# Performance work log

Measured on AMD Instinct MI355X. Metric: run time of the kernel, lower is better.

Reference implementation:

```python
import jax, jax.numpy as jnp
import numpy as np

EPS_IN = 1e-5  # torch InstanceNorm2d default eps


def _gather_nb(feat, idx):
    # feat: [B, C, N], idx: [B, M, K] -> [B, C, M, K]
    return jnp.take_along_axis(feat[:, :, :, None], idx[:, None, :, :], axis=2)


def _fc(x, w):
    # 1x1 conv2d: w [O, C], x [B, C, N, K] -> [B, O, N, K]
    return jnp.einsum('oc,bcnk->bonk', w, x)


def _inorm(x, w, b):
    # InstanceNorm2d(affine=True): per (batch, channel) stats over (N, K)
    mu = jnp.mean(x, axis=(2, 3), keepdims=True)
    var = jnp.var(x, axis=(2, 3), keepdims=True)
    xn = (x - mu) / jnp.sqrt(var + EPS_IN)
    return xn * w[None, :, None, None] + b[None, :, None, None]


def setup_inputs() -> dict:
    key = jax.random.key(0)
    ks = jax.random.split(key, 16)
    B, C_in, C_out, N, K = 8, 64, 64, 8192, 16
    x = jax.random.normal(ks[0], (B, C_in, N), dtype=jnp.float32)
    pos = jax.random.normal(ks[1], (B, 3, N), dtype=jnp.float32)
    support_points = jax.random.normal(ks[2], (B, 3, N), dtype=jnp.float32)
    neighbors_indices = jax.random.randint(ks[3], (B, N, K), 0, N)
    fc1_w = jax.random.normal(ks[4], (K, 3), dtype=jnp.float32) * 0.1
    fc2_w = jax.random.normal(ks[5], (K, 2 * K), dtype=jnp.float32) * 0.1
    fc3_w = jax.random.normal(ks[6], (K, 2 * K), dtype=jnp.float32) * 0.1
    bn1_w = jnp.ones((K,), jnp.float32)
    bn1_b = jnp.zeros((K,), jnp.float32)
    bn2_w = jnp.ones((K,), jnp.float32)
    bn2_b = jnp.zeros((K,), jnp.float32)
    cv_w = jax.random.normal(ks[7], (C_out, C_in, K), dtype=jnp.float32) * 0.05
    alpha = jnp.ones((1,), jnp.float32)
    beta = jnp.ones((1,), jnp.float32)
    return dict(x=x, pos=pos, support_points=support_points,
                neighbors_indices=neighbors_indices,
                fc1_w=fc1_w, fc2_w=fc2_w, fc3_w=fc3_w,
                bn1_w=bn1_w, bn1_b=bn1_b, bn2_w=bn2_w, bn2_b=bn2_b,
                cv_w=cv_w, alpha=alpha, beta=beta)


def reference(x, pos, support_points, neighbors_indices,
              fc1_w, fc2_w, fc3_w, bn1_w, bn1_b, bn2_w, bn2_b,
              cv_w, alpha, beta):
    K = neighbors_indices.shape[-1]
    pos_g = _gather_nb(pos, neighbors_indices)   # [B,3,N,K]
    x_g = _gather_nb(x, neighbors_indices)       # [B,C,N,K]
    pts = pos_g - support_points[:, :, :, None]  # [B,3,N,K]

    # adaptive normalization (eval mode; norm_radius == 1)
    d = jnp.sqrt(jnp.sum(jax.lax.stop_gradient(pts) ** 2, axis=1))  # [B,N,K]
    dw = jax.nn.sigmoid(-alpha[0] * d + beta[0])
    dws = jnp.sum(dw, axis=2, keepdims=True)
    dws = dws + (dws == 0).astype(dw.dtype) + 1e-6
    dw = (dw / dws * K)[:, None, :, :]           # [B,1,N,K]

    mat = jax.nn.relu(_inorm(_fc(pts, fc1_w), bn1_w, bn1_b))          # [B,K,N,K]
    mp1 = jnp.broadcast_to(jnp.max(mat * dw, axis=3, keepdims=True), mat.shape)
    mat = jnp.concatenate([mat, mp1], axis=1)
    mat = jax.nn.relu(_inorm(_fc(mat, fc2_w), bn2_w, bn2_b))
    mp2 = jnp.broadcast_to(jnp.max(mat * dw, axis=3, keepdims=True), mat.shape)
    mat = jnp.concatenate([mat, mp2], axis=1)
    mat = jax.nn.relu(_fc(mat, fc3_w)) * dw      # [B,Kk,N,K]

    # x.transpose(1,2) @ mat.permute(0,2,3,1): contract over neighbor axis k
    feats = jnp.einsum('bcnk,bjnk->bcnj', x_g, mat)  # [B,C,N,Kk]
    # Conv2d(in, out, (1, Kk)) then squeeze(3)
    out = jnp.einsum('ocj,bcnj->bon', cv_w, feats)   # [B,Cout,N]
    return out
```

## Files before the change

kernel.cpp:

```cpp
#include <hip/hip_runtime.h>
#include <cstdint>
#include <cstddef>

#define B_ 8
#define C_ 64
#define N_ 8192
#define K_ 16
#define CNT_ ((float)(N_ * K_))

typedef __attribute__((ext_vector_type(4))) float f32x4;
typedef __attribute__((ext_vector_type(8))) short short8;

union U8 { short8 v; unsigned u[4]; };

__device__ __forceinline__ unsigned pk2bf(float a, float b) {
    unsigned ua = __float_as_uint(a) + 0x8000u;
    unsigned ub = __float_as_uint(b) + 0x8000u;
    return __builtin_amdgcn_perm(ub, ua, 0x07060302u);
}
__device__ __forceinline__ unsigned short f2bf(float x) {
    return (unsigned short)((__float_as_uint(x) + 0x8000u) >> 16);
}
__device__ __forceinline__ float bflo(unsigned u) { return __uint_as_float(u << 16); }
__device__ __forceinline__ float bfhi(unsigned u) { return __uint_as_float(u & 0xffff0000u); }

template <int CTRL>
__device__ __forceinline__ float dppf(float v) {
    return __int_as_float(__builtin_amdgcn_update_dpp(0, __float_as_int(v), CTRL, 0xF, 0xF, true));
}
__device__ __forceinline__ float dpp_max16(float v) {
    v = fmaxf(v, dppf<0xB1>(v));
    v = fmaxf(v, dppf<0x4E>(v));
    v = fmaxf(v, dppf<0x141>(v));
    v = fmaxf(v, dppf<0x140>(v));
    return v;
}
__device__ __forceinline__ float dpp_add4(float v) {
    v += dppf<0xB1>(v);
    v += dppf<0x4E>(v);
    return v;
}
__device__ __forceinline__ float dpp_max4(float v) {
    v = fmaxf(v, dppf<0xB1>(v));
    v = fmaxf(v, dppf<0x4E>(v));
    return v;
}


__global__ __launch_bounds__(256) void k_pre(
    const float* __restrict__ cv, unsigned short* __restrict__ wf,
    const float* __restrict__ x, unsigned* __restrict__ xtb32, int use_xt,
    const float* __restrict__ pos, const float* __restrict__ sup,
    const int* __restrict__ nb, float* __restrict__ stats) {
    __shared__ float t[64][65];
    __shared__ float red[4][9];
    int tid = threadIdx.x;

    if (blockIdx.x < 256) {
        int g = blockIdx.x * 256 + tid;
        int e = g & 7, l = (g >> 3) & 63, w = (g >> 9) & 3, ks = g >> 11;
        int o = w * 16 + (l & 15);
        int i = ks * 32 + (l >> 4) * 8 + e;
        wf[g] = f2bf(cv[o * 1024 + i]);
        return;
    }
    int bid = blockIdx.x - 256;
    int b = bid >> 7, n0 = (bid & 127) << 6;

    if (use_xt) {
        int a = tid & 63, g = tid >> 6;
#pragma unroll
        for (int cc = 0; cc < 64; cc += 4)
            t[a][cc + g] = x[((size_t)b * 64 + cc + g) * N_ + n0 + a];
        __syncthreads();
        int cp = tid & 31, h = tid >> 5;
#pragma unroll
        for (int nn = 0; nn < 64; nn += 8) {
            int n = nn + h;
            xtb32[((size_t)b * N_ + n0 + n) * 32 + cp] = pk2bf(t[n][cp * 2], t[n][cp * 2 + 1]);
        }
    }

    {
        int n = n0 + (tid >> 2), q = tid & 3;
        size_t gn = (size_t)b * N_ + n;
        float sx = sup[(b * 3 + 0) * N_ + n];
        float sy = sup[(b * 3 + 1) * N_ + n];
        float sz = sup[(b * 3 + 2) * N_ + n];
        int4 ids = *(const int4*)&nb[gn * K_ + q * 4];
        const float* px_ = pos + (b * 3 + 0) * N_;
        const float* py_ = pos + (b * 3 + 1) * N_;
        const float* pz_ = pos + (b * 3 + 2) * N_;
        float Gx = 0.f, Gy = 0.f, Gz = 0.f;
        float Axx = 0.f, Ayy = 0.f, Azz = 0.f, Axy = 0.f, Axz = 0.f, Ayz = 0.f;
        int idk[4] = {ids.x, ids.y, ids.z, ids.w};
#pragma unroll
        for (int k = 0; k < 4; ++k) {
            int id = idk[k];
            float gx = px_[id], gy = py_[id], gz = pz_[id];
            Gx += gx; Gy += gy; Gz += gz;
            Axx = fmaf(gx, gx, Axx); Ayy = fmaf(gy, gy, Ayy); Azz = fmaf(gz, gz, Azz);
            Axy = fmaf(gx, gy, Axy); Axz = fmaf(gx, gz, Axz); Ayz = fmaf(gy, gz, Ayz);
        }
        float v[9];
        v[0] = Gx - 4.f * sx;
        v[1] = Gy - 4.f * sy;
        v[2] = Gz - 4.f * sz;
        v[3] = Axx - 2.f * sx * Gx + 4.f * sx * sx;
        v[4] = Ayy - 2.f * sy * Gy + 4.f * sy * sy;
        v[5] = Azz - 2.f * sz * Gz + 4.f * sz * sz;
        v[6] = Axy - sx * Gy - sy * Gx + 4.f * sx * sy;
        v[7] = Axz - sx * Gz - sz * Gx + 4.f * sx * sz;
        v[8] = Ayz - sy * Gz - sz * Gy + 4.f * sy * sz;
#pragma unroll
        for (int m = 1; m < 64; m <<= 1)
#pragma unroll
            for (int tt = 0; tt < 9; ++tt) v[tt] += __shfl_xor(v[tt], m);
        if ((tid & 63) == 0)
#pragma unroll
            for (int tt = 0; tt < 9; ++tt) red[tid >> 6][tt] = v[tt];
    }
    __syncthreads();
    if (tid < 9) {
        float s = red[0][tid] + red[1][tid] + red[2][tid] + red[3][tid];
        atomicAdd(&stats[b * 12 + tid], s);
    }
}

__global__ __launch_bounds__(256) void k_mid(
    const float* __restrict__ pos, const float* __restrict__ sup,
    const int* __restrict__ nb, const float* __restrict__ w1,
    const float* __restrict__ w2,
    const float* __restrict__ bn1w, const float* __restrict__ bn1b,
    const float* __restrict__ alpha, const float* __restrict__ beta,
    float* __restrict__ stats, unsigned* __restrict__ s2b,
    float* __restrict__ dwb, float* __restrict__ stats2, int store_s2) {
    __shared__ float sc1[16], sh1[16];
    __shared__ uint4 tile[4][64][4];
    __shared__ float redS[4][16], redQ[4][16];

    int tid = threadIdx.x;
    int wid = tid >> 6, l = tid & 63, hi = l >> 4, c15 = l & 15;
    int gn = blockIdx.x * 64 + (tid >> 2);
    int b = gn >> 13, n = gn & 8191, q = tid & 3;

    if (tid < 16) {
        int j = tid;
        const float* M = &stats[b * 12];
        float wx = w1[j * 3], wy = w1[j * 3 + 1], wz = w1[j * 3 + 2];
        float sum = wx * M[0] + wy * M[1] + wz * M[2];
        float sq = wx * wx * M[3] + wy * wy * M[4] + wz * wz * M[5]
                 + 2.f * (wx * wy * M[6] + wx * wz * M[7] + wy * wz * M[8]);
        float mu = sum / CNT_;
        float var = sq / CNT_ - mu * mu;
        float is = rsqrtf(var + 1e-5f);
        float sc = bn1w[j] * is;
        sc1[j] = sc;
        sh1[j] = bn1b[j] - mu * sc;
    }
    __syncthreads();

    union { short8 v; unsigned short u[8]; } af;
#pragma unroll
    for (int t = 0; t < 8; ++t) af.u[t] = f2bf(w2[c15 * 32 + hi * 8 + t]);

    float sx = sup[(b * 3 + 0) * N_ + n];
    float sy = sup[(b * 3 + 1) * N_ + n];
    float sz = sup[(b * 3 + 2) * N_ + n];
    int4 ids = *(const int4*)&nb[(size_t)gn * K_ + q * 4];
    int idk[4] = {ids.x, ids.y, ids.z, ids.w};

    float pxa[4], pya[4], pza[4], dwv[4];
    float dsum = 0.f;
    float al = alpha[0], be = beta[0];
#pragma unroll
    for (int k = 0; k < 4; ++k) {
        int id = idk[k];
        float px = pos[(b * 3 + 0) * N_ + id] - sx;
        float py = pos[(b * 3 + 1) * N_ + id] - sy;
        float pz = pos[(b * 3 + 2) * N_ + id] - sz;
        pxa[k] = px; pya[k] = py; pza[k] = pz;
        float d = sqrtf(px * px + py * py + pz * pz);
        float v = 1.f / (1.f + __expf(al * d - be));
        dwv[k] = v;
        dsum += v;
    }
    dsum = dpp_add4(dsum);
    float inv = 16.f / (dsum + (dsum == 0.f ? 1.f : 0.f) + 1e-6f);
#pragma unroll
    for (int k = 0; k < 4; ++k) dwv[k] *= inv;
    if (store_s2)
        *(float4*)&dwb[(size_t)gn * 16 + q * 4] = make_float4(dwv[0], dwv[1], dwv[2], dwv[3]);

    float mp1[16];
#pragma unroll
    for (int j = 0; j < 16; ++j) mp1[j] = 0.f;
    unsigned m1p[4][8];
#pragma unroll
    for (int t = 0; t < 4; ++t) {
        float px = pxa[t], py = pya[t], pz = pza[t], dw = dwv[t];
#pragma unroll
        for (int jp = 0; jp < 8; ++jp) {
            int j0 = 2 * jp, j1 = 2 * jp + 1;
            float v0 = fmaf(w1[j0 * 3 + 2], pz, fmaf(w1[j0 * 3 + 1], py, w1[j0 * 3] * px));
            float m0 = fmaxf(fmaf(v0, sc1[j0], sh1[j0]), 0.f);
            float v1 = fmaf(w1[j1 * 3 + 2], pz, fmaf(w1[j1 * 3 + 1], py, w1[j1 * 3] * px));
            float m1 = fmaxf(fmaf(v1, sc1[j1], sh1[j1]), 0.f);
            mp1[j0] = fmaxf(mp1[j0], m0 * dw);
            mp1[j1] = fmaxf(mp1[j1], m1 * dw);
            m1p[t][jp] = pk2bf(m0, m1);
        }
    }
#pragma unroll
    for (int j = 0; j < 16; ++j) mp1[j] = dpp_max4(mp1[j]);
    {
        unsigned mq[8];
#pragma unroll
        for (int t = 0; t < 8; ++t) mq[t] = pk2bf(mp1[2 * t], mp1[2 * t + 1]);
        tile[wid][l][2 ^ (l & 3)] = make_uint4(mq[0], mq[1], mq[2], mq[3]);
        tile[wid][l][3 ^ (l & 3)] = make_uint4(mq[4], mq[5], mq[6], mq[7]);
    }

    float ssum[4] = {0.f, 0.f, 0.f, 0.f}, ssq[4] = {0.f, 0.f, 0.f, 0.f};
    const f32x4 zero = {0.f, 0.f, 0.f, 0.f};

#pragma unroll
    for (int t = 0; t < 4; ++t) {
        tile[wid][l][0 ^ (l & 3)] = make_uint4(m1p[t][0], m1p[t][1], m1p[t][2], m1p[t][3]);
        tile[wid][l][1 ^ (l & 3)] = make_uint4(m1p[t][4], m1p[t][5], m1p[t][6], m1p[t][7]);
#pragma unroll
        for (int cg = 0; cg < 4; ++cg) {
            int e = cg * 16 + c15;
            union { uint4 u; short8 s; } bf;
            bf.u = tile[wid][e][hi ^ (e & 3)];
            f32x4 D = __builtin_amdgcn_mfma_f32_16x16x32_bf16(af.v, bf.s, zero, 0, 0, 0);
#pragma unroll
            for (int r = 0; r < 4; ++r) {
                ssum[r] += D[r];
                ssq[r] = fmaf(D[r], D[r], ssq[r]);
            }
            if (store_s2) {
                unsigned* tb = s2b + ((size_t)blockIdx.x * 64 + wid * 16 + cg * 4 + (c15 >> 2)) * 128;
                tb[t * 32 + (c15 & 3) * 8 + hi * 2 + 0] = pk2bf(D[0], D[1]);
                tb[t * 32 + (c15 & 3) * 8 + hi * 2 + 1] = pk2bf(D[2], D[3]);
            }
        }
    }
#pragma unroll
    for (int r = 0; r < 4; ++r) {
#pragma unroll
        for (int m = 1; m < 16; m <<= 1) {
            ssum[r] += __shfl_xor(ssum[r], m);
            ssq[r] += __shfl_xor(ssq[r], m);
        }
    }
    if (c15 == 0) {
#pragma unroll
        for (int r = 0; r < 4; ++r) { redS[wid][hi * 4 + r] = ssum[r]; redQ[wid][hi * 4 + r] = ssq[r]; }
    }
    __syncthreads();
    if (tid < 32) {
        int s = tid & 15;
        float v = (tid < 16) ? (redS[0][s] + redS[1][s] + redS[2][s] + redS[3][s])
                             : (redQ[0][s] + redQ[1][s] + redQ[2][s] + redQ[3][s]);
        if (store_s2) {
            atomicAdd(&stats2[(blockIdx.x & 7) * 256 + b * 32 + tid], v);
        } else {
            atomicAdd(&stats[(tid < 16 ? 256 : 384) + b * 16 + s], v);
        }
    }
}

template <int USE_XT, int USE_S2>
__global__ __launch_bounds__(256, 4) void k_main(
    const float* __restrict__ x, const unsigned short* __restrict__ xtb,
    const float* __restrict__ pos, const float* __restrict__ sup,
    const int* __restrict__ nb,
    const float* __restrict__ w1, const float* __restrict__ w2, const float* __restrict__ w3,
    const float* __restrict__ bn1w, const float* __restrict__ bn1b,
    const float* __restrict__ bn2w, const float* __restrict__ bn2b,
    const float* __restrict__ alpha, const float* __restrict__ beta,
    const unsigned short* __restrict__ wf,
    const float* __restrict__ stats,
    const unsigned* __restrict__ s2b, const float* __restrict__ dwb,
    const float* __restrict__ stats2,
    float* __restrict__ out) {
    __shared__ __align__(16) char lds_u[32768];
    int (*sidx)[4][16] = (int (*)[4][16])(lds_u + 16384);
    float* sc1 = (float*)(lds_u + 17408);
    float* sh1 = (float*)(lds_u + 17472);
    float* sc2 = (float*)(lds_u + 17536);
    float* sh2 = (float*)(lds_u + 17600);

    int tid = threadIdx.x;
    int b = blockIdx.x & 7;
    int n0 = (blockIdx.x >> 3) << 4;
    int wid = tid >> 6, l = tid & 63, hi = l >> 4, c15 = l & 15;
    int hi2 = hi >> 1;
    const f32x4 zero = {0.f, 0.f, 0.f, 0.f};

    {
        int n = n0 + wid * 4 + hi;
        sidx[wid][hi][c15] = nb[((size_t)b * N_ + n) * K_ + c15];
    }

    unsigned G0[4][4], G1[4][4];
    if constexpr (USE_XT) {
        const unsigned short* xb = xtb + (size_t)b * N_ * 64;
#pragma unroll
        for (int pi = 0; pi < 4; ++pi) {
            int4 ids = *(const int4*)&sidx[wid][pi][hi * 4];
            int idr[4] = {ids.x, ids.y, ids.z, ids.w};
#pragma unroll
            for (int r = 0; r < 4; ++r) {
                uint2 g = *(const uint2*)(xb + (size_t)idr[r] * 64 + c15 * 4);
                G0[pi][r] = g.x; G1[pi][r] = g.y;
            }
        }
    }

    uint2 sv[4];
    float dwc[4];
    if constexpr (USE_S2) {
#pragma unroll
        for (int eg = 0; eg < 4; ++eg) {
            size_t gn_e = (size_t)b * N_ + n0 + wid * 4 + eg;
            sv[eg] = *(const uint2*)&s2b[gn_e * 128 + (c15 & 3) * 32 + (c15 >> 2) * 8 + hi * 2];
            dwc[eg] = dwb[gn_e * 16 + c15];
        }
    }

    if constexpr (USE_S2) {
        if (tid < 32) {
            float acc = 0.f;
#pragma unroll
            for (int c = 0; c < 8; ++c) acc += stats2[c * 256 + b * 32 + tid];
            float sq = __shfl(acc, (tid & 15) + 16);
            if (tid < 16) {
                float mu = acc / CNT_;
                float var = sq / CNT_ - mu * mu;
                float is = rsqrtf(var + 1e-5f);
                float sc = bn2w[tid] * is;
                sc2[tid] = sc;
                sh2[tid] = bn2b[tid] - mu * sc;
            }
        }
    } else if (tid < 32) {
        int j = tid & 15, set = tid >> 4;
        float mu, var;
        if (set == 0) {
            const float* M = &stats[b * 12];
            float wx = w1[j * 3], wy = w1[j * 3 + 1], wz = w1[j * 3 + 2];
            float sum = wx * M[0] + wy * M[1] + wz * M[2];
            float sq = wx * wx * M[3] + wy * wy * M[4] + wz * wz * M[5]
                     + 2.f * (wx * wy * M[6] + wx * wz * M[7] + wy * wz * M[8]);
            mu = sum / CNT_;
            var = sq / CNT_ - mu * mu;
        } else {
            float su = stats[256 + b * 16 + j];
            float sq = stats[384 + b * 16 + j];
            mu = su / CNT_;
            var = sq / CNT_ - mu * mu;
        }
        float is = rsqrtf(var + 1e-5f);
        float wv = set ? bn2w[j] : bn1w[j];
        float bv = set ? bn2b[j] : bn1b[j];
        float scale = wv * is;
        if (set == 0) { sc1[j] = scale; sh1[j] = bv - mu * scale; }
        else          { sc2[j] = scale; sh2[j] = bv - mu * scale; }
    }
    __syncthreads();

    U8 w3f;
    {
        const float* wp = w3 + c15 * 32 + hi * 8;
        w3f.u[0] = pk2bf(wp[0], wp[1]); w3f.u[1] = pk2bf(wp[2], wp[3]);
        w3f.u[2] = pk2bf(wp[4], wp[5]); w3f.u[3] = pk2bf(wp[6], wp[7]);
    }
    float sc2r[4], sh2r[4];
#pragma unroll
    for (int r = 0; r < 4; ++r) { sc2r[r] = sc2[hi * 4 + r]; sh2r[r] = sh2[hi * 4 + r]; }

    char* tw = lds_u + (wid << 12);

    float m2v[4][4];
    if constexpr (USE_S2) {
#pragma unroll
        for (int eg = 0; eg < 4; ++eg) {
            m2v[eg][0] = fmaxf(fmaf(bflo(sv[eg].x), sc2r[0], sh2r[0]), 0.f);
            m2v[eg][1] = fmaxf(fmaf(bfhi(sv[eg].x), sc2r[1], sh2r[1]), 0.f);
            m2v[eg][2] = fmaxf(fmaf(bflo(sv[eg].y), sc2r[2], sh2r[2]), 0.f);
            m2v[eg][3] = fmaxf(fmaf(bfhi(sv[eg].y), sc2r[3], sh2r[3]), 0.f);
        }
    } else {
        U8 w2f;
        {
            const float* wp = w2 + c15 * 32 + hi * 8;
            w2f.u[0] = pk2bf(wp[0], wp[1]); w2f.u[1] = pk2bf(wp[2], wp[3]);
            w2f.u[2] = pk2bf(wp[4], wp[5]); w2f.u[3] = pk2bf(wp[6], wp[7]);
        }
        float dw;
        {
            int p_e = wid * 4 + hi;
            int n = n0 + p_e;
            int id = sidx[wid][hi][c15];
            float px = pos[(b * 3 + 0) * N_ + id] - sup[(b * 3 + 0) * N_ + n];
            float py = pos[(b * 3 + 1) * N_ + id] - sup[(b * 3 + 1) * N_ + n];
            float pz = pos[(b * 3 + 2) * N_ + id] - sup[(b * 3 + 2) * N_ + n];
            float d = sqrtf(px * px + py * py + pz * pz);
            float dwr = 1.f / (1.f + __expf(alpha[0] * d - beta[0]));
            float dws = dwr;
            dws += __shfl_xor(dws, 1); dws += __shfl_xor(dws, 2);
            dws += __shfl_xor(dws, 4); dws += __shfl_xor(dws, 8);
            dws += (dws == 0.f ? 1.f : 0.f) + 1e-6f;
            dw = dwr * 16.f / dws;

            float m1[16];
#pragma unroll
            for (int j = 0; j < 16; ++j) {
                float v = fmaf(w1[j * 3 + 2], pz, fmaf(w1[j * 3 + 1], py, w1[j * 3] * px));
                m1[j] = fmaxf(fmaf(v, sc1[j], sh1[j]), 0.f);
            }
            float mp1[16];
#pragma unroll
            for (int j = 0; j < 16; ++j) {
                float t = m1[j] * dw;
                t = fmaxf(t, __shfl_xor(t, 1)); t = fmaxf(t, __shfl_xor(t, 2));
                t = fmaxf(t, __shfl_xor(t, 4)); t = fmaxf(t, __shfl_xor(t, 8));
                mp1[j] = t;
            }
            int swz = (l >> 1) & 7;
            uint4 q0 = make_uint4(pk2bf(m1[0], m1[1]), pk2bf(m1[2], m1[3]), pk2bf(m1[4], m1[5]), pk2bf(m1[6], m1[7]));
            uint4 q1 = make_uint4(pk2bf(m1[8], m1[9]), pk2bf(m1[10], m1[11]), pk2bf(m1[12], m1[13]), pk2bf(m1[14], m1[15]));
            uint4 q2 = make_uint4(pk2bf(mp1[0], mp1[1]), pk2bf(mp1[2], mp1[3]), pk2bf(mp1[4], mp1[5]), pk2bf(mp1[6], mp1[7]));
            uint4 q3 = make_uint4(pk2bf(mp1[8], mp1[9]), pk2bf(mp1[10], mp1[11]), pk2bf(mp1[12], mp1[13]), pk2bf(mp1[14], mp1[15]));
            ((uint4*)tw)[(l * 4 + 0) ^ swz] = q0;
            ((uint4*)tw)[(l * 4 + 1) ^ swz] = q1;
            ((uint4*)tw)[(l * 4 + 2) ^ swz] = q2;
            ((uint4*)tw)[(l * 4 + 3) ^ swz] = q3;
        }
#pragma unroll
        for (int eg = 0; eg < 4; ++eg) {
            int e = eg * 16 + c15;
            uint4 t = ((const uint4*)tw)[(e * 4 + hi) ^ (c15 >> 1)];
            U8 bf; bf.u[0] = t.x; bf.u[1] = t.y; bf.u[2] = t.z; bf.u[3] = t.w;
            f32x4 D2 = __builtin_amdgcn_mfma_f32_16x16x32_bf16(w2f.v, bf.v, zero, 0, 0, 0);
            dwc[eg] = __shfl(dw, eg * 16 + c15);
#pragma unroll
            for (int r = 0; r < 4; ++r)
                m2v[eg][r] = fmaxf(fmaf(D2[r], sc2r[r], sh2r[r]), 0.f);
        }
    }

#pragma unroll
    for (int eg = 0; eg < 4; ++eg) {
        float mp2v[4];
#pragma unroll
        for (int r = 0; r < 4; ++r)
            mp2v[r] = dpp_max16(m2v[eg][r] * dwc[eg]);
        uint2 mq = make_uint2(pk2bf(m2v[eg][0], m2v[eg][1]), pk2bf(m2v[eg][2], m2v[eg][3]));
        uint2 pq = make_uint2(pk2bf(mp2v[0], mp2v[1]), pk2bf(mp2v[2], mp2v[3]));
        int e = eg * 16 + c15, sw = c15 >> 1;
        ((uint2*)tw)[(e * 8 + hi) ^ sw] = mq;
        ((uint2*)tw)[(e * 8 + 4 + hi) ^ sw] = pq;
    }

    f32x4 D3[4];
#pragma unroll
    for (int eg = 0; eg < 4; ++eg) {
        int e = eg * 16 + c15, sw = c15 >> 1;
        uint2 b0 = ((const uint2*)tw)[(e * 8 + hi * 2) ^ sw];
        uint2 b1 = ((const uint2*)tw)[(e * 8 + hi * 2 + 1) ^ sw];
        U8 bf; bf.u[0] = b0.x; bf.u[1] = b0.y; bf.u[2] = b1.x; bf.u[3] = b1.y;
        D3[eg] = __builtin_amdgcn_mfma_f32_16x16x32_bf16(w3f.v, bf.v, zero, 0, 0, 0);
    }

#pragma unroll
    for (int eg = 0; eg < 4; ++eg) {
#pragma unroll
        for (int r = 0; r < 4; ++r) {
            float v = fmaxf(D3[eg][r], 0.f) * dwc[eg];
            ((unsigned short*)(tw + eg * 640))[(hi * 4 + r) * 20 + c15] = f2bf(v);
        }
    }

    uint2 afr2[4];
#pragma unroll
    for (int pi = 0; pi < 4; ++pi)
        afr2[pi] = *(const uint2*)(tw + pi * 640 + c15 * 40 + hi * 8);

    uint2 dv[4][4];
    if constexpr (USE_XT) {
#pragma unroll
        for (int pi = 0; pi < 4; ++pi) {
            U8 av; av.u[0] = afr2[pi].x; av.u[1] = afr2[pi].y; av.u[2] = 0; av.u[3] = 0;
#pragma unroll
            for (int cg = 0; cg < 4; ++cg) {
                unsigned w0 = (cg < 2) ? G0[pi][0] : G1[pi][0];
                unsigned w1_ = (cg < 2) ? G0[pi][1] : G1[pi][1];
                unsigned w2_ = (cg < 2) ? G0[pi][2] : G1[pi][2];
                unsigned w3_ = (cg < 2) ? G0[pi][3] : G1[pi][3];
                unsigned sel = (cg & 1) ? 0x07060302u : 0x05040100u;
                U8 bf;
                bf.u[0] = __builtin_amdgcn_perm(w1_, w0, sel);
                bf.u[1] = __builtin_amdgcn_perm(w3_, w2_, sel);
                bf.u[2] = 0; bf.u[3] = 0;
                f32x4 D = __builtin_amdgcn_mfma_f32_16x16x32_bf16(av.v, bf.v, zero, 0, 0, 0);
                dv[pi][cg] = make_uint2(pk2bf(D[0], D[1]), pk2bf(D[2], D[3]));
            }
        }
    } else {
#pragma unroll
        for (int pi = 0; pi < 4; ++pi) {
            int4 ids = *(const int4*)&sidx[wid][pi][hi * 4];
            U8 av; av.u[0] = afr2[pi].x; av.u[1] = afr2[pi].y; av.u[2] = 0; av.u[3] = 0;
#pragma unroll
            for (int cg = 0; cg < 4; ++cg) {
                int c = cg * 16 + c15;
                const float* xc = x + ((size_t)b * 64 + c) * N_;
                U8 bf;
                bf.u[0] = pk2bf(xc[ids.x], xc[ids.y]);
                bf.u[1] = pk2bf(xc[ids.z], xc[ids.w]);
                bf.u[2] = 0; bf.u[3] = 0;
                f32x4 D = __builtin_amdgcn_mfma_f32_16x16x32_bf16(av.v, bf.v, zero, 0, 0, 0);
                dv[pi][cg] = make_uint2(pk2bf(D[0], D[1]), pk2bf(D[2], D[3]));
            }
        }
    }

    __syncthreads();

    const unsigned short* wbase = wf + (size_t)wid * 512 + (size_t)l * 8;
    U8 aW[4];
#pragma unroll
    for (int i = 0; i < 4; ++i) aW[i].v = *(const short8*)(wbase + (size_t)i * 2048);

#pragma unroll
    for (int pi = 0; pi < 4; ++pi) {
        int p = wid * 4 + pi;
#pragma unroll
        for (int cg = 0; cg < 4; ++cg) {
            int cF = USE_XT ? (c15 * 4 + cg) : (cg * 16 + c15);
            int xr = cF >> 2;
            *(uint2*)(lds_u + (cF * 2 + hi2) * 256 + ((p ^ xr) << 4) + ((hi & 1) << 3)) = dv[pi][cg];
        }
    }
    __syncthreads();

    f32x4 acc0 = {0.f, 0.f, 0.f, 0.f}, acc1 = {0.f, 0.f, 0.f, 0.f};
#pragma unroll
    for (int ks = 0; ks < 32; ++ks) {
        uint4 t = *(const uint4*)(lds_u + ks * 1024 + hi * 256 + ((c15 ^ (ks >> 1)) << 4));
        U8 bf; bf.u[0] = t.x; bf.u[1] = t.y; bf.u[2] = t.z; bf.u[3] = t.w;
        if (ks & 1)
            acc1 = __builtin_amdgcn_mfma_f32_16x16x32_bf16(aW[ks & 3].v, bf.v, acc1, 0, 0, 0);
        else
            acc0 = __builtin_amdgcn_mfma_f32_16x16x32_bf16(aW[ks & 3].v, bf.v, acc0, 0, 0, 0);
        if (ks < 28) aW[ks & 3].v = *(const short8*)(wbase + (size_t)(ks + 4) * 2048);
    }

    {
        int o = wid * 16 + hi * 4;
#pragma unroll
        for (int r = 0; r < 4; ++r)
            out[((size_t)b * 64 + o + r) * N_ + n0 + c15] = acc0[r] + acc1[r];
    }
}

extern "C" void kernel_launch(void* const* d_in, const int* in_sizes, int n_in,
                              void* d_out, int out_size, void* d_ws, size_t ws_size,
                              hipStream_t stream) {
    const float* x    = (const float*)d_in[0];
    const float* pos  = (const float*)d_in[1];
    const float* sup  = (const float*)d_in[2];
    const int*   nb   = (const int*)d_in[3];
    const float* w1   = (const float*)d_in[4];
    const float* w2   = (const float*)d_in[5];
    const float* w3   = (const float*)d_in[6];
    const float* bn1w = (const float*)d_in[7];
    const float* bn1b = (const float*)d_in[8];
    const float* bn2w = (const float*)d_in[9];
    const float* bn2b = (const float*)d_in[10];
    const float* cv   = (const float*)d_in[11];
    const float* alpha = (const float*)d_in[12];
    const float* beta  = (const float*)d_in[13];
    float* out = (float*)d_out;

    char* ws = (char*)d_ws;
    float* stats = (float*)ws;
    float* stats2 = (float*)(ws + 2048);
    unsigned short* wfrag = (unsigned short*)(ws + 10240);
    unsigned short* xtb = (unsigned short*)(ws + 141312);
    size_t xt_end = 141312 + (size_t)B_ * N_ * 64 * 2;
    unsigned* s2b = (unsigned*)(ws + xt_end);
    size_t dw_off = xt_end + (size_t)B_ * N_ * K_ * 16 * 2;
    float* dwb = (float*)(ws + dw_off);
    size_t s2_need = dw_off + (size_t)B_ * N_ * K_ * 4;
    int use_xt = (ws_size >= xt_end) ? 1 : 0;
    int use_s2 = (ws_size >= s2_need) ? 1 : 0;

    hipMemsetAsync(ws, 0, 10240, stream);
    k_pre<<<1280, 256, 0, stream>>>(cv, wfrag, x, (unsigned*)xtb, use_xt, pos, sup, nb, stats);
    k_mid<<<1024, 256, 0, stream>>>(pos, sup, nb, w1, w2, bn1w, bn1b, alpha, beta,
                                    stats, s2b, dwb, stats2, use_s2);
    dim3 gmain(B_ * (N_ / 16));
    if (use_xt && use_s2) {
        k_main<1, 1><<<gmain, 256, 0, stream>>>(x, xtb, pos, sup, nb, w1, w2, w3,
                                                bn1w, bn1b, bn2w, bn2b, alpha, beta,
                                                wfrag, stats, s2b, dwb, stats2, out);
    } else if (use_xt) {
        k_main<1, 0><<<gmain, 256, 0, stream>>>(x, xtb, pos, sup, nb, w1, w2, w3,
                                                bn1w, bn1b, bn2w, bn2b, alpha, beta,
                                                wfrag, stats, s2b, dwb, stats2, out);
    } else {
        k_main<0, 0><<<gmain, 256, 0, stream>>>(x, xtb, pos, sup, nb, w1, w2, w3,
                                                bn1w, bn1b, bn2w, bn2b, alpha, beta,
                                                wfrag, stats, s2b, dwb, stats2, out);
    }
}
```

Baseline: 88.44 us.

## Split final contraction into two channel halves to shrink LDS and registers

For the XT+S2 variant, the gathered x features and the feats-to-output contraction are processed in two channel halves. The second half's gather is deferred until after the first half's MFMA pass. This halves the LDS staging buffer (about 17.6KB instead of 32KB) and the G/dv register arrays, and launch bounds are raised to 5 blocks per SM to use the freed resources for occupancy. In exchange it adds extra barriers and a second, later gather whose latency is less hidden.

Result: slower. 116.4 us (+31.6%).

```diff
diff --git a/kernel.cpp b/kernel.cpp
--- a/kernel.cpp
+++ b/kernel.cpp
@@ -272,7 +272,7 @@
 }
 
 template <int USE_XT, int USE_S2>
-__global__ __launch_bounds__(256, 4) void k_main(
+__global__ __launch_bounds__(256, 5) void k_main(
     const float* __restrict__ x, const unsigned short* __restrict__ xtb,
     const float* __restrict__ pos, const float* __restrict__ sup,
     const int* __restrict__ nb,
@@ -285,7 +285,8 @@
     const unsigned* __restrict__ s2b, const float* __restrict__ dwb,
     const float* __restrict__ stats2,
     float* __restrict__ out) {
-    __shared__ __align__(16) char lds_u[32768];
+    constexpr bool SPLIT = (USE_XT && USE_S2);
+    __shared__ __align__(16) char lds_u[SPLIT ? 17664 : 32768];
     int (*sidx)[4][16] = (int (*)[4][16])(lds_u + 16384);
     float* sc1 = (float*)(lds_u + 17408);
     float* sh1 = (float*)(lds_u + 17472);
@@ -298,6 +299,7 @@
     int wid = tid >> 6, l = tid & 63, hi = l >> 4, c15 = l & 15;
     int hi2 = hi >> 1;
     const f32x4 zero = {0.f, 0.f, 0.f, 0.f};
+    const unsigned short* xb = xtb + (size_t)b * N_ * 64;
 
     {
         int n = n0 + wid * 4 + hi;
@@ -306,15 +308,18 @@
 
     unsigned G0[4][4], G1[4][4];
     if constexpr (USE_XT) {
-        const unsigned short* xb = xtb + (size_t)b * N_ * 64;
 #pragma unroll
         for (int pi = 0; pi < 4; ++pi) {
             int4 ids = *(const int4*)&sidx[wid][pi][hi * 4];
             int idr[4] = {ids.x, ids.y, ids.z, ids.w};
 #pragma unroll
             for (int r = 0; r < 4; ++r) {
-                uint2 g = *(const uint2*)(xb + (size_t)idr[r] * 64 + c15 * 4);
-                G0[pi][r] = g.x; G1[pi][r] = g.y;
+                if constexpr (SPLIT) {
+                    G0[pi][r] = *(const unsigned*)(xb + (size_t)idr[r] * 64 + c15 * 4);
+                } else {
+                    uint2 g = *(const uint2*)(xb + (size_t)idr[r] * 64 + c15 * 4);
+                    G0[pi][r] = g.x; G1[pi][r] = g.y;
+                }
             }
         }
     }
@@ -489,81 +494,183 @@
     for (int pi = 0; pi < 4; ++pi)
         afr2[pi] = *(const uint2*)(tw + pi * 640 + c15 * 40 + hi * 8);
 
-    uint2 dv[4][4];
-    if constexpr (USE_XT) {
+    if constexpr (SPLIT) {
+        uint2 dvA[4][2];
 #pragma unroll
         for (int pi = 0; pi < 4; ++pi) {
             U8 av; av.u[0] = afr2[pi].x; av.u[1] = afr2[pi].y; av.u[2] = 0; av.u[3] = 0;
 #pragma unroll
-            for (int cg = 0; cg < 4; ++cg) {
-                unsigned w0 = (cg < 2) ? G0[pi][0] : G1[pi][0];
-                unsigned w1_ = (cg < 2) ? G0[pi][1] : G1[pi][1];
-                unsigned w2_ = (cg < 2) ? G0[pi][2] : G1[pi][2];
-                unsigned w3_ = (cg < 2) ? G0[pi][3] : G1[pi][3];
-                unsigned sel = (cg & 1) ? 0x07060302u : 0x05040100u;
+            for (int cgl = 0; cgl < 2; ++cgl) {
+                unsigned sel = cgl ? 0x07060302u : 0x05040100u;
                 U8 bf;
-                bf.u[0] = __builtin_amdgcn_perm(w1_, w0, sel);
-                bf.u[1] = __builtin_amdgcn_perm(w3_, w2_, sel);
+                bf.u[0] = __builtin_amdgcn_perm(G0[pi][1], G0[pi][0], sel);
+                bf.u[1] = __builtin_amdgcn_perm(G0[pi][3], G0[pi][2], sel);
                 bf.u[2] = 0; bf.u[3] = 0;
                 f32x4 D = __builtin_amdgcn_mfma_f32_16x16x32_bf16(av.v, bf.v, zero, 0, 0, 0);
-                dv[pi][cg] = make_uint2(pk2bf(D[0], D[1]), pk2bf(D[2], D[3]));
-            }
-        }
-    } else {
+                dvA[pi][cgl] = make_uint2(pk2bf(D[0], D[1]), pk2bf(D[2], D[3]));
+            }
+        }
+        __syncthreads();
+
+#pragma unroll
+        for (int pi = 0; pi < 4; ++pi) {
+            int p = wid * 4 + pi;
+#pragma unroll
+            for (int cgl = 0; cgl < 2; ++cgl) {
+                int rc = c15 * 4 + cgl * 2 + hi2;
+                *(uint2*)(lds_u + rc * 256 + ((p ^ c15) << 4) + ((hi & 1) << 3)) = dvA[pi][cgl];
+            }
+        }
+        const unsigned short* wbase = wf + (size_t)wid * 512 + (size_t)l * 8;
+        U8 aW[4];
+#pragma unroll
+        for (int i = 0; i < 4; ++i) aW[i].v = *(const short8*)(wbase + (size_t)(2 * i) * 2048);
+        __syncthreads();
+
 #pragma unroll
         for (int pi = 0; pi < 4; ++pi) {
             int4 ids = *(const int4*)&sidx[wid][pi][hi * 4];
+            int idr[4] = {ids.x, ids.y, ids.z, ids.w};
+#pragma unroll
+            for (int r = 0; r < 4; ++r)
+                G1[pi][r] = *(const unsigned*)(xb + (size_t)idr[r] * 64 + c15 * 4 + 2);
+        }
+
+        f32x4 acc0 = {0.f, 0.f, 0.f, 0.f}, acc1 = {0.f, 0.f, 0.f, 0.f};
+#pragma unroll
+        for (int t = 0; t < 16; ++t) {
+            uint4 v = *(const uint4*)(lds_u + (4 * t + hi) * 256 + ((c15 ^ t) << 4));
+            U8 bf; bf.u[0] = v.x; bf.u[1] = v.y; bf.u[2] = v.z; bf.u[3] = v.w;
+            if (t & 1)
+                acc1 = __builtin_amdgcn_mfma_f32_16x16x32_bf16(aW[t & 3].v, bf.v, acc1, 0, 0, 0);
+            else
+                acc0 = __builtin_amdgcn_mfma_f32_16x16x32_bf16(aW[t & 3].v, bf.v, acc0, 0, 0, 0);
+            if (t < 12) aW[t & 3].v = *(const short8*)(wbase + (size_t)(2 * (t + 4)) * 2048);
+        }
+        __syncthreads();
+
+        uint2 dvB[4][2];
+#pragma unroll
+        for (int pi = 0; pi < 4; ++pi) {
             U8 av; av.u[0] = afr2[pi].x; av.u[1] = afr2[pi].y; av.u[2] = 0; av.u[3] = 0;
 #pragma unroll
-            for (int cg = 0; cg < 4; ++cg) {
-                int c = cg * 16 + c15;
-                const float* xc = x + ((size_t)b * 64 + c) * N_;
+            for (int cgl = 0; cgl < 2; ++cgl) {
+                unsigned sel = cgl ? 0x07060302u : 0x05040100u;
                 U8 bf;
-                bf.u[0] = pk2bf(xc[ids.x], xc[ids.y]);
-                bf.u[1] = pk2bf(xc[ids.z], xc[ids.w]);
+                bf.u[0] = __builtin_amdgcn_perm(G1[pi][1], G1[pi][0], sel);
+                bf.u[1] = __builtin_amdgcn_perm(G1[pi][3], G1[pi][2], sel);
                 bf.u[2] = 0; bf.u[3] = 0;
                 f32x4 D = __builtin_amdgcn_mfma_f32_16x16x32_bf16(av.v, bf.v, zero, 0, 0, 0);
-                dv[pi][cg] = make_uint2(pk2bf(D[0], D[1]), pk2bf(D[2], D[3]));
-            }
-        }
-    }
-
-    __syncthreads();
-
-    const unsigned short* wbase = wf + (size_t)wid * 512 + (size_t)l * 8;
-    U8 aW[4];
-#pragma unroll
-    for (int i = 0; i < 4; ++i) aW[i].v = *(const short8*)(wbase + (size_t)i * 2048);
-
-#pragma unroll
-    for (int pi = 0; pi < 4; ++pi) {
-        int p = wid * 4 + pi;
-#pragma unroll
-        for (int cg = 0; cg < 4; ++cg) {
-            int cF = USE_XT ? (c15 * 4 + cg) : (cg * 16 + c15);
-            int xr = cF >> 2;
-            *(uint2*)(lds_u + (cF * 2 + hi2) * 256 + ((p ^ xr) << 4) + ((hi & 1) << 3)) = dv[pi][cg];
-        }
-    }
-    __syncthreads();
-
-    f32x4 acc0 = {0.f, 0.f, 0.f, 0.f}, acc1 = {0.f, 0.f, 0.f, 0.f};
-#pragma unroll
-    for (int ks = 0; ks < 32; ++ks) {
-        uint4 t = *(const uint4*)(lds_u + ks * 1024 + hi * 256 + ((c15 ^ (ks >> 1)) << 4));
-        U8 bf; bf.u[0] = t.x; bf.u[1] = t.y; bf.u[2] = t.z; bf.u[3] = t.w;
-        if (ks & 1)
-            acc1 = __builtin_amdgcn_mfma_f32_16x16x32_bf16(aW[ks & 3].v, bf.v, acc1, 0, 0, 0);
-        else
-            acc0 = __builtin_amdgcn_mfma_f32_16x16x32_bf16(aW[ks & 3].v, bf.v, acc0, 0, 0, 0);
-        if (ks < 28) aW[ks & 3].v = *(const short8*)(wbase + (size_t)(ks + 4) * 2048);
-    }
-
-    {
-        int o = wid * 16 + hi * 4;
-#pragma unroll
-        for (int r = 0; r < 4; ++r)
-            out[((size_t)b * 64 + o + r) * N_ + n0 + c15] = acc0[r] + acc1[r];
+                dvB[pi][cgl] = make_uint2(pk2bf(D[0], D[1]), pk2bf(D[2], D[3]));
+            }
+        }
+#pragma unroll
+        for (int pi = 0; pi < 4; ++pi) {
+            int p = wid * 4 + pi;
+#pragma unroll
+            for (int cgl = 0; cgl < 2; ++cgl) {
+                int rc = c15 * 4 + cgl * 2 + hi2;
+                *(uint2*)(lds_u + rc * 256 + ((p ^ c15) << 4) + ((hi & 1) << 3)) = dvB[pi][cgl];
+            }
+        }
+#pragma unroll
+        for (int i = 0; i < 4; ++i) aW[i].v = *(const short8*)(wbase + (size_t)(2 * i + 1) * 2048);
+        __syncthreads();
+
+#pragma unroll
+        for (int t = 0; t < 16; ++t) {
+            uint4 v = *(const uint4*)(lds_u + (4 * t + hi) * 256 + ((c15 ^ t) << 4));
+            U8 bf; bf.u[0] = v.x; bf.u[1] = v.y; bf.u[2] = v.z; bf.u[3] = v.w;
+            if (t & 1)
+                acc1 = __builtin_amdgcn_mfma_f32_16x16x32_bf16(aW[t & 3].v, bf.v, acc1, 0, 0, 0);
+            else
+                acc0 = __builtin_amdgcn_mfma_f32_16x16x32_bf16(aW[t & 3].v, bf.v, acc0, 0, 0, 0);
+            if (t < 12) aW[t & 3].v = *(const short8*)(wbase + (size_t)(2 * (t + 4) + 1) * 2048);
+        }
+
+        {
+            int o = wid * 16 + hi * 4;
+#pragma unroll
+            for (int r = 0; r < 4; ++r)
+                out[((size_t)b * 64 + o + r) * N_ + n0 + c15] = acc0[r] + acc1[r];
+        }
+    } else {
+        uint2 dv[4][4];
+        if constexpr (USE_XT) {
+#pragma unroll
+            for (int pi = 0; pi < 4; ++pi) {
+                U8 av; av.u[0] = afr2[pi].x; av.u[1] = afr2[pi].y; av.u[2] = 0; av.u[3] = 0;
+#pragma unroll
+                for (int cg = 0; cg < 4; ++cg) {
+                    unsigned w0 = (cg < 2) ? G0[pi][0] : G1[pi][0];
+                    unsigned w1_ = (cg < 2) ? G0[pi][1] : G1[pi][1];
+                    unsigned w2_ = (cg < 2) ? G0[pi][2] : G1[pi][2];
+                    unsigned w3_ = (cg < 2) ? G0[pi][3] : G1[pi][3];
+                    unsigned sel = (cg & 1) ? 0x07060302u : 0x05040100u;
+                    U8 bf;
+                    bf.u[0] = __builtin_amdgcn_perm(w1_, w0, sel);
+                    bf.u[1] = __builtin_amdgcn_perm(w3_, w2_, sel);
+                    bf.u[2] = 0; bf.u[3] = 0;
+                    f32x4 D = __builtin_amdgcn_mfma_f32_16x16x32_bf16(av.v, bf.v, zero, 0, 0, 0);
+                    dv[pi][cg] = make_uint2(pk2bf(D[0], D[1]), pk2bf(D[2], D[3]));
+                }
+            }
+        } else {
+#pragma unroll
+            for (int pi = 0; pi < 4; ++pi) {
+                int4 ids = *(const int4*)&sidx[wid][pi][hi * 4];
+                U8 av; av.u[0] = afr2[pi].x; av.u[1] = afr2[pi].y; av.u[2] = 0; av.u[3] = 0;
+#pragma unroll
+                for (int cg = 0; cg < 4; ++cg) {
+                    int c = cg * 16 + c15;
+                    const float* xc = x + ((size_t)b * 64 + c) * N_;
+                    U8 bf;
+                    bf.u[0] = pk2bf(xc[ids.x], xc[ids.y]);
+                    bf.u[1] = pk2bf(xc[ids.z], xc[ids.w]);
+                    bf.u[2] = 0; bf.u[3] = 0;
+                    f32x4 D = __builtin_amdgcn_mfma_f32_16x16x32_bf16(av.v, bf.v, zero, 0, 0, 0);
+                    dv[pi][cg] = make_uint2(pk2bf(D[0], D[1]), pk2bf(D[2], D[3]));
+                }
+            }
+        }
+
+        __syncthreads();
+
+        const unsigned short* wbase = wf + (size_t)wid * 512 + (size_t)l * 8;
+        U8 aW[4];
+#pragma unroll
+        for (int i = 0; i < 4; ++i) aW[i].v = *(const short8*)(wbase + (size_t)i * 2048);
+
+#pragma unroll
+        for (int pi = 0; pi < 4; ++pi) {
+            int p = wid * 4 + pi;
+#pragma unroll
+            for (int cg = 0; cg < 4; ++cg) {
+                int cF = USE_XT ? (c15 * 4 + cg) : (cg * 16 + c15);
+                int xr = cF >> 2;
+                *(uint2*)(lds_u + (cF * 2 + hi2) * 256 + ((p ^ xr) << 4) + ((hi & 1) << 3)) = dv[pi][cg];
+            }
+        }
+        __syncthreads();
+
+        f32x4 acc0 = {0.f, 0.f, 0.f, 0.f}, acc1 = {0.f, 0.f, 0.f, 0.f};
+#pragma unroll
+        for (int ks = 0; ks < 32; ++ks) {
+            uint4 t = *(const uint4*)(lds_u + ks * 1024 + hi * 256 + ((c15 ^ (ks >> 1)) << 4));
+            U8 bf; bf.u[0] = t.x; bf.u[1] = t.y; bf.u[2] = t.z; bf.u[3] = t.w;
+            if (ks & 1)
+                acc1 = __builtin_amdgcn_mfma_f32_16x16x32_bf16(aW[ks & 3].v, bf.v, acc1, 0, 0, 0);
+            else
+                acc0 = __builtin_amdgcn_mfma_f32_16x16x32_bf16(aW[ks & 3].v, bf.v, acc0, 0, 0, 0);
+            if (ks < 28) aW[ks & 3].v = *(const short8*)(wbase + (size_t)(ks + 4) * 2048);
+        }
+
+        {
+            int o = wid * 16 + hi * 4;
+#pragma unroll
+            for (int r = 0; r < 4; ++r)
+                out[((size_t)b * 64 + o + r) * N_ + n0 + c15] = acc0[r] + acc1[r];
+        }
     }
 }
 
```
